# Kernel optimization log

Measured on AMD Instinct MI355X. Metric: run time of the kernel, lower is better.

## Reference

```python
import jax, jax.numpy as jnp
import numpy as np

B, C, H, W = 2, 320, 48, 48
HEADS, DIM_HEAD, NUM_FILTERS = 8, 64, 32
INNER = HEADS * DIM_HEAD  # 512
LN_EPS = 1e-05


def setup_inputs() -> dict:
    key = jax.random.key(0)
    ks = jax.random.split(key, 8)
    w = 0.02
    return {
        "hidden_states": jax.random.normal(ks[0], (B, C, H, W), jnp.float32),
        "encoder_hidden_states": jax.random.normal(ks[1], (B, C, H, W), jnp.float32),
        "Wq": jax.random.normal(ks[2], (C, INNER), jnp.float32) * w,
        "Wk": jax.random.normal(ks[3], (C, INNER), jnp.float32) * w,
        "Wv": jax.random.normal(ks[4], (C, INNER), jnp.float32) * w,
        "Wo": jax.random.normal(ks[5], (INNER, C), jnp.float32) * w,
        "bo": jnp.zeros((C,), jnp.float32),
        "ln_gamma": jnp.ones((C,), jnp.float32),
        "ln_beta": jnp.zeros((C,), jnp.float32),
        "ex_filters": jax.random.normal(ks[6], (NUM_FILTERS, INNER), jnp.float32),
        "dist_filters": jax.random.normal(ks[7], (NUM_FILTERS, INNER), jnp.float32),
        "scale": jnp.ones((1,), jnp.float32),  # learnable scale shadows dim_head**-0.5
    }


def _split_heads(t, heads):
    b, s, d = t.shape
    return t.reshape(b, s, heads, d // heads).transpose(0, 2, 1, 3)  # [b,h,s,dh]


def reference(hidden_states, encoder_hidden_states, Wq, Wk, Wv, Wo, bo,
              ln_gamma, ln_beta, ex_filters, dist_filters, scale):
    b, c, h, w = hidden_states.shape
    _, _, rh, rw = encoder_hidden_states.shape
    residual = hidden_states
    s = scale[0]

    hs = hidden_states.transpose(0, 2, 3, 1).reshape(b, h * w, c)        # [b, q, C]
    ehs = encoder_hidden_states.transpose(0, 2, 3, 1).reshape(b, rh * rw, c)

    # LayerNorm on encoder states
    mu = ehs.mean(-1, keepdims=True)
    var = jnp.mean((ehs - mu) ** 2, axis=-1, keepdims=True)
    ehs = (ehs - mu) * jax.lax.rsqrt(var + LN_EPS) * ln_gamma + ln_beta

    q = _split_heads(hs @ Wq, HEADS)    # [b,h,q,dh]
    k = _split_heads(ehs @ Wk, HEADS)   # [b,h,kv,dh]
    v = _split_heads(ehs @ Wv, HEADS)   # [b,h,kv,dh]
    ef = _split_heads(jnp.broadcast_to(ex_filters[None], (b,) + ex_filters.shape), HEADS)   # [b,h,F,dh]
    df = _split_heads(jnp.broadcast_to(dist_filters[None], (b,) + dist_filters.shape), HEADS)

    # spatial attention: softmax over kv positions
    spatial = jax.nn.softmax(jnp.einsum('bhfd,bhkd->bhfk', ef, k) * s, axis=-1)   # [b,h,F,kv]
    # channel attention: softmax over the filter axis (torch dim=1 of [B*h, F, q])
    channel = jax.nn.softmax(jnp.einsum('bhfd,bhqd->bhfq', df, q) * s, axis=2)    # [b,h,F,q]

    attn = jnp.einsum('bhfq,bhfk->bhqk', channel, spatial)                        # [b,h,q,kv]
    out = jnp.einsum('bhqk,bhkd->bhqd', attn, v)                                  # [b,h,q,dh]

    out = out.transpose(0, 2, 1, 3).reshape(b, h * w, INNER)
    out = out @ Wo + bo
    out = out.reshape(b, h, w, c).transpose(0, 3, 1, 2)
    return out + residual * s
```

## Files before the change

kernel.cpp:

```cpp
#include <hip/hip_runtime.h>
#include <math.h>

#define Bc 2
#define Cc 320
#define Pc 2304
#define HEADSc 8
#define DHc 64
#define INNERc 512
#define Fc 32
#define LN_EPS 1e-5f
#define CHUNKS 18
#define CHUNK_P 128

typedef __attribute__((ext_vector_type(8))) short bf16x8;
typedef __attribute__((ext_vector_type(4))) float f32x4;

static __device__ __forceinline__ ushort f2bf(float x) {
  uint u = __builtin_bit_cast(uint, x);
  u = (u + 0x7fffu + ((u >> 16) & 1u)) >> 16;
  return (ushort)u;
}

static __device__ __forceinline__ void gload16(const ushort* g, ushort* l) {
  __builtin_amdgcn_global_load_lds(
      (const __attribute__((address_space(1))) uint*)g,
      (__attribute__((address_space(3))) uint*)l, 16, 0, 0);
}

static __device__ void transpose_tile(const float* __restrict__ src,
                                      ushort* __restrict__ dst, int R, int C,
                                      int r0, int c0, int tid,
                                      float (*t)[65]) {
#pragma unroll
  for (int it = 0; it < 4; ++it) {
    int lin = it * 256 + tid;
    int rr = lin >> 4, c4 = lin & 15;
    float4 v = *(const float4*)(&src[(size_t)(r0 + rr) * C + c0 + c4 * 4]);
    t[rr][c4 * 4 + 0] = v.x; t[rr][c4 * 4 + 1] = v.y;
    t[rr][c4 * 4 + 2] = v.z; t[rr][c4 * 4 + 3] = v.w;
  }
  __syncthreads();
#pragma unroll
  for (int it = 0; it < 2; ++it) {
    int lin = it * 256 + tid;
    int cc = lin >> 3, r8 = lin & 7;
    ushort tmp[8];
#pragma unroll
    for (int j = 0; j < 8; ++j) tmp[j] = f2bf(t[r8 * 8 + j][cc]);
    *(uint4*)(&dst[(size_t)(c0 + cc) * R + r0 + r8 * 8]) = *(const uint4*)tmp;
  }
}

__global__ __launch_bounds__(256) void prep_all_kernel(
    const float* __restrict__ hs, const float* __restrict__ ehs,
    const float* __restrict__ gamma, const float* __restrict__ beta,
    const float* __restrict__ Wv, const float* __restrict__ Wo,
    const float* __restrict__ exf, const float* __restrict__ Wk,
    const float* __restrict__ dif, const float* __restrict__ Wq,
    ushort* __restrict__ hsT, ushort* __restrict__ ehsT,
    ushort* __restrict__ WvT, ushort* __restrict__ WoT,
    ushort* __restrict__ Gk, ushort* __restrict__ Gq) {
  __shared__ float smem[6448];
  int idx = blockIdx.x, tid = threadIdx.x;

  if (idx < 144) {
    int pt = idx % 36, z = idx / 36;
    int b = z & 1, which = z >> 1;
    int pos0 = pt * 64;
    const float* src = (which ? ehs : hs) + (size_t)b * Cc * Pc;
    ushort* dst = (which ? ehsT : hsT) + (size_t)b * Pc * Cc;
    float* t = smem;
    float* s1 = smem + 4160;
    float* s2 = smem + 4416;
    float* lmean = smem + 4672;
    float* lrstd = smem + 4736;
    int lane = tid & 63, g = tid >> 6;
    if (which) {
      const float* base = src + pos0 + lane;
      float sum = 0.f, sq = 0.f;
      for (int c = g * 80; c < g * 80 + 80; ++c) {
        float x = base[(size_t)c * Pc];
        sum += x; sq += x * x;
      }
      s1[g * 64 + lane] = sum; s2[g * 64 + lane] = sq;
      __syncthreads();
      if (tid < 64) {
        float ts = s1[tid] + s1[64 + tid] + s1[128 + tid] + s1[192 + tid];
        float tq = s2[tid] + s2[64 + tid] + s2[128 + tid] + s2[192 + tid];
        float mean = ts / (float)Cc;
        float var = tq / (float)Cc - mean * mean;
        lmean[tid] = mean;
        lrstd[tid] = rsqrtf(var + LN_EPS);
      }
      __syncthreads();
    }
    for (int ct = 0; ct < 5; ++ct) {
      int r0 = ct * 64;
#pragma unroll
      for (int it = 0; it < 4; ++it) {
        int lin = it * 256 + tid;
        int rr = lin >> 4, c4 = lin & 15;
        float4 v = *(const float4*)(&src[(size_t)(r0 + rr) * Pc + pos0 + c4 * 4]);
        t[rr * 65 + c4 * 4 + 0] = v.x; t[rr * 65 + c4 * 4 + 1] = v.y;
        t[rr * 65 + c4 * 4 + 2] = v.z; t[rr * 65 + c4 * 4 + 3] = v.w;
      }
      __syncthreads();
#pragma unroll
      for (int it = 0; it < 2; ++it) {
        int lin = it * 256 + tid;
        int cc = lin >> 3, r8 = lin & 7;
        float m_ = which ? lmean[cc] : 0.f, rs_ = which ? lrstd[cc] : 1.f;
        ushort tmp[8];
#pragma unroll
        for (int j = 0; j < 8; ++j) {
          int ch = r8 * 8 + j;
          float x = t[ch * 65 + cc];
          float val = which ? (x - m_) * rs_ * gamma[r0 + ch] + beta[r0 + ch] : x;
          tmp[j] = f2bf(val);
        }
        *(uint4*)(&dst[(size_t)(pos0 + cc) * Cc + r0 + r8 * 8]) =
            *(const uint4*)tmp;
      }
      __syncthreads();
    }
  } else {
    int idx2 = idx - 144;
    if (idx2 < 40) {
      transpose_tile(Wv, WvT, Cc, INNERc, (idx2 / 8) * 64, (idx2 % 8) * 64,
                     tid, (float(*)[65])smem);
    } else if (idx2 < 80) {
      int i = idx2 - 40;
      transpose_tile(Wo, WoT, INNERc, Cc, (i / 5) * 64, (i % 5) * 64, tid,
                     (float(*)[65])smem);
    } else {
      int i = idx2 - 80;
      int c0 = (i % 5) * 64, h = (i / 5) % 8, zz = i / 40;
      const float* filt = zz ? dif : exf;
      const float* W = zz ? Wq : Wk;
      ushort* G = zz ? Gq : Gk;
      float (*ef)[66] = (float(*)[66])smem;
      float (*wk)[65] = (float(*)[65])(smem + 32 * 66);
      for (int l = tid; l < Fc * DHc; l += 256) {
        int f = l >> 6, d = l & 63;
        ef[f][d] = filt[(size_t)f * INNERc + h * 64 + d];
      }
      for (int l = tid; l < 64 * DHc; l += 256) {
        int cc = l >> 6, d = l & 63;
        wk[cc][d] = W[(size_t)(c0 + cc) * INNERc + h * 64 + d];
      }
      __syncthreads();
      int f = tid >> 3, cbase = tid & 7;
      float acc[8] = {};
#pragma unroll
      for (int d4 = 0; d4 < DHc; d4 += 4) {
        float4 a = *(const float4*)(&ef[f][d4]);
#pragma unroll
        for (int j = 0; j < 8; ++j) {
          float4 b = *(const float4*)(&wk[cbase + j * 8][d4]);
          acc[j] += a.x * b.x + a.y * b.y + a.z * b.z + a.w * b.w;
        }
      }
#pragma unroll
      for (int j = 0; j < 8; ++j)
        G[(size_t)(h * Fc + f) * Cc + c0 + cbase + j * 8] = f2bf(acc[j]);
    }
  }
}

__global__ __launch_bounds__(256) void spatial_kernel(
    const ushort* __restrict__ Gk, const ushort* __restrict__ ehsT,
    const ushort* __restrict__ WvT, const float* __restrict__ scale_p,
    float* __restrict__ svp, float* __restrict__ mj, float* __restrict__ lj) {
  int c = blockIdx.x, h = blockIdx.y, b = blockIdx.z;
  int tid = threadIdx.x, lane = tid & 63, wv = tid >> 6;
  int l15 = lane & 15, kq = lane >> 4;
  int pos0 = c * CHUNK_P;
  int bh = b * HEADSc + h;
  float s = scale_p[0];

  __shared__ alignas(16) ushort As[96 * 64];
  __shared__ alignas(16) ushort Bs[128 * 64];
  __shared__ float Sq[32 * 132];
  __shared__ alignas(16) ushort P[32 * 136];
  __shared__ alignas(16) ushort Vs[64 * 136];

  const ushort* Av = WvT + (size_t)(h * 64) * Cc;
  const ushort* Ag = Gk + (size_t)(h * Fc) * Cc;
  const ushort* Bb = ehsT + ((size_t)b * Pc + pos0) * Cc;

  f32x4 acc[6][2] = {};
  for (int k0 = 0; k0 < Cc; k0 += 64) {
#pragma unroll
    for (int it = 0; it < 3; ++it) {
      int lin = it * 256 + tid;
      int row = lin >> 3, p = lin & 7;
      int lc = p ^ (row & 7);
      const ushort* sp = (row < 64) ? (Av + (size_t)row * Cc + k0 + lc * 8)
                                    : (Ag + (size_t)(row - 64) * Cc + k0 + lc * 8);
      gload16(sp, &As[lin * 8]);
    }
#pragma unroll
    for (int it = 0; it < 4; ++it) {
      int lin = it * 256 + tid;
      int row = lin >> 3, p = lin & 7;
      int lc = p ^ (row & 7);
      gload16(Bb + (size_t)row * Cc + k0 + lc * 8, &Bs[lin * 8]);
    }
    __syncthreads();
#pragma unroll
    for (int ss = 0; ss < 2; ++ss) {
      bf16x8 af[6], bfr[2];
#pragma unroll
      for (int mt = 0; mt < 6; ++mt) {
        int m = mt * 16 + l15;
        int p = (ss * 4 + kq) ^ (m & 7);
        af[mt] = *(const bf16x8*)(&As[m * 64 + p * 8]);
      }
#pragma unroll
      for (int nt = 0; nt < 2; ++nt) {
        int n = wv * 32 + nt * 16 + l15;
        int p = (ss * 4 + kq) ^ (n & 7);
        bfr[nt] = *(const bf16x8*)(&Bs[n * 64 + p * 8]);
      }
#pragma unroll
      for (int mt = 0; mt < 6; ++mt)
#pragma unroll
        for (int nt = 0; nt < 2; ++nt)
          acc[mt][nt] = __builtin_amdgcn_mfma_f32_16x16x32_bf16(
              af[mt], bfr[nt], acc[mt][nt], 0, 0, 0);
    }
    __syncthreads();
  }
#pragma unroll
  for (int mt = 0; mt < 6; ++mt)
#pragma unroll
    for (int nt = 0; nt < 2; ++nt) {
      int col = wv * 32 + nt * 16 + l15;
#pragma unroll
      for (int r = 0; r < 4; ++r) {
        int row = mt * 16 + kq * 4 + r;
        if (mt < 4) Vs[row * 136 + col] = f2bf(acc[mt][nt][r]);
        else Sq[(row - 64) * 132 + col] = acc[mt][nt][r];
      }
    }
  __syncthreads();

  {
    int row = tid >> 3, sub = tid & 7;
    float vals[16];
    float m_ = -1e30f;
#pragma unroll
    for (int i = 0; i < 16; ++i) {
      vals[i] = s * Sq[row * 132 + sub * 16 + i];
      m_ = fmaxf(m_, vals[i]);
    }
    m_ = fmaxf(m_, __shfl_xor(m_, 1));
    m_ = fmaxf(m_, __shfl_xor(m_, 2));
    m_ = fmaxf(m_, __shfl_xor(m_, 4));
    float l_ = 0.f;
#pragma unroll
    for (int i = 0; i < 16; i += 2) {
      float e0 = __expf(vals[i] - m_);
      float e1 = __expf(vals[i + 1] - m_);
      l_ += e0 + e1;
      uint pk = (uint)f2bf(e0) | ((uint)f2bf(e1) << 16);
      *(uint*)(&P[row * 136 + sub * 16 + i]) = pk;
    }
    l_ += __shfl_xor(l_, 1);
    l_ += __shfl_xor(l_, 2);
    l_ += __shfl_xor(l_, 4);
    if (sub == 0) {
      mj[((size_t)c * 16 + bh) * Fc + row] = m_;
      lj[((size_t)c * 16 + bh) * Fc + row] = l_;
    }
  }
  __syncthreads();

  f32x4 acc2[2] = {};
#pragma unroll
  for (int ss = 0; ss < 4; ++ss) {
    bf16x8 af[2];
#pragma unroll
    for (int mt = 0; mt < 2; ++mt)
      af[mt] = *(const bf16x8*)(&P[(mt * 16 + l15) * 136 + ss * 32 + kq * 8]);
    bf16x8 bfr = *(const bf16x8*)(&Vs[(wv * 16 + l15) * 136 + ss * 32 + kq * 8]);
#pragma unroll
    for (int mt = 0; mt < 2; ++mt)
      acc2[mt] = __builtin_amdgcn_mfma_f32_16x16x32_bf16(af[mt], bfr, acc2[mt],
                                                         0, 0, 0);
  }
  float* op = svp + ((size_t)c * 16 + bh) * (Fc * DHc);
#pragma unroll
  for (int mt = 0; mt < 2; ++mt)
#pragma unroll
    for (int r = 0; r < 4; ++r)
      op[(mt * 16 + kq * 4 + r) * DHc + wv * 16 + l15] = acc2[mt][r];
}

__global__ __launch_bounds__(256) void sv_reduce_kernel(
    const float* __restrict__ svp, const float* __restrict__ mj,
    const float* __restrict__ lj, ushort* __restrict__ svT) {
  int idx = blockIdx.x * 256 + threadIdx.x;
  int d = idx & 63, fr = idx >> 6;
  int bh = fr >> 5, f = fr & 31;
  float m = -1e30f;
#pragma unroll
  for (int c = 0; c < CHUNKS; ++c)
    m = fmaxf(m, mj[((size_t)c * 16 + bh) * Fc + f]);
  float osum = 0.f, lsum = 0.f;
#pragma unroll
  for (int c = 0; c < CHUNKS; ++c) {
    float w = __expf(mj[((size_t)c * 16 + bh) * Fc + f] - m);
    osum += w * svp[((size_t)c * 16 + bh) * (Fc * DHc) + f * DHc + d];
    lsum += w * lj[((size_t)c * 16 + bh) * Fc + f];
  }
  svT[((size_t)bh * DHc + d) * Fc + f] = f2bf(osum / lsum);
}

__global__ __launch_bounds__(256) void channel_kernel(
    const ushort* __restrict__ Gq, const ushort* __restrict__ hsT,
    const ushort* __restrict__ svT, const float* __restrict__ scale_p,
    ushort* __restrict__ OAT) {
  int pb = blockIdx.x, hp = blockIdx.y, b = blockIdx.z;
  int pos0 = pb * 64;
  int tid = threadIdx.x, lane = tid & 63, wv = tid >> 6;
  int l15 = lane & 15, kq = lane >> 4;
  float s = scale_p[0];

  __shared__ alignas(16) ushort Aq[2 * 32 * 64];
  __shared__ alignas(16) ushort Bs[64 * 64];
  __shared__ float SO[64 * 68];
  __shared__ alignas(16) ushort Pt[64 * 40];
  __shared__ alignas(16) ushort svs[64 * 40];
  __shared__ float red[4 * 64];

  f32x4 acc[2][2] = {};
  const ushort* Bb = hsT + ((size_t)b * Pc + pos0) * Cc;
  for (int k0 = 0; k0 < Cc; k0 += 64) {
#pragma unroll
    for (int it = 0; it < 2; ++it) {
      int lin = it * 256 + tid;
      int hh = lin >> 8, row = (lin >> 3) & 31, p = lin & 7;
      int lc = p ^ (row & 7);
      gload16(Gq + (size_t)((hp * 2 + hh) * Fc + row) * Cc + k0 + lc * 8,
              &Aq[lin * 8]);
    }
#pragma unroll
    for (int it = 0; it < 2; ++it) {
      int lin = it * 256 + tid;
      int row = lin >> 3, p = lin & 7;
      int lc = p ^ (row & 7);
      gload16(Bb + (size_t)row * Cc + k0 + lc * 8, &Bs[lin * 8]);
    }
    __syncthreads();
#pragma unroll
    for (int ss = 0; ss < 2; ++ss) {
      int n = wv * 16 + l15;
      int pb_ = (ss * 4 + kq) ^ (n & 7);
      bf16x8 bfr = *(const bf16x8*)(&Bs[n * 64 + pb_ * 8]);
#pragma unroll
      for (int hh = 0; hh < 2; ++hh)
#pragma unroll
        for (int mt = 0; mt < 2; ++mt) {
          int m = mt * 16 + l15;
          int pa = (ss * 4 + kq) ^ (m & 7);
          bf16x8 af = *(const bf16x8*)(&Aq[hh * 2048 + m * 64 + pa * 8]);
          acc[hh][mt] = __builtin_amdgcn_mfma_f32_16x16x32_bf16(
              af, bfr, acc[hh][mt], 0, 0, 0);
        }
    }
    __syncthreads();
  }

  for (int hh = 0; hh < 2; ++hh) {
    int h = hp * 2 + hh;
#pragma unroll
    for (int mt = 0; mt < 2; ++mt)
#pragma unroll
      for (int r = 0; r < 4; ++r)
        SO[(mt * 16 + kq * 4 + r) * 68 + wv * 16 + l15] = acc[hh][mt][r];
    {
      int rr = tid >> 2, p = tid & 3;
      *(uint4*)(&svs[rr * 40 + p * 8]) = *(const uint4*)(
          svT + ((size_t)(b * HEADSc + h) * DHc + rr) * Fc + p * 8);
    }
    __syncthreads();
    {
      int pos = tid & 63, g = tid >> 6;
      float v8[8];
      float pm = -1e30f;
#pragma unroll
      for (int i = 0; i < 8; ++i) {
        v8[i] = s * SO[(g * 8 + i) * 68 + pos];
        pm = fmaxf(pm, v8[i]);
      }
      red[g * 64 + pos] = pm;
      __syncthreads();
      float m_ = fmaxf(fmaxf(red[pos], red[64 + pos]),
                       fmaxf(red[128 + pos], red[192 + pos]));
      __syncthreads();
      float ps = 0.f;
#pragma unroll
      for (int i = 0; i < 8; ++i) {
        v8[i] = __expf(v8[i] - m_);
        ps += v8[i];
      }
      red[g * 64 + pos] = ps;
      __syncthreads();
      float inv = 1.f / (red[pos] + red[64 + pos] + red[128 + pos] +
                         red[192 + pos]);
#pragma unroll
      for (int i = 0; i < 8; i += 2) {
        uint pk = (uint)f2bf(v8[i] * inv) | ((uint)f2bf(v8[i + 1] * inv) << 16);
        *(uint*)(&Pt[pos * 40 + g * 8 + i]) = pk;
      }
    }
    __syncthreads();
    {
      bf16x8 b_ = *(const bf16x8*)(&svs[(wv * 16 + l15) * 40 + kq * 8]);
      f32x4 acc3[4];
#pragma unroll
      for (int mt = 0; mt < 4; ++mt) {
        bf16x8 a_ = *(const bf16x8*)(&Pt[(mt * 16 + l15) * 40 + kq * 8]);
        f32x4 z = {0.f, 0.f, 0.f, 0.f};
        acc3[mt] = __builtin_amdgcn_mfma_f32_16x16x32_bf16(a_, b_, z, 0, 0, 0);
      }
#pragma unroll
      for (int mt = 0; mt < 4; ++mt)
#pragma unroll
        for (int r = 0; r < 4; ++r)
          SO[(mt * 16 + kq * 4 + r) * 68 + wv * 16 + l15] = acc3[mt][r];
    }
    __syncthreads();
#pragma unroll
    for (int it = 0; it < 2; ++it) {
      int lin = it * 256 + tid;
      int p = lin >> 3, c8 = lin & 7;
      ushort tmp[8];
#pragma unroll
      for (int j = 0; j < 8; ++j) tmp[j] = f2bf(SO[p * 68 + c8 * 8 + j]);
      *(uint4*)(&OAT[((size_t)b * Pc + pos0 + p) * INNERc + h * 64 + c8 * 8]) =
          *(const uint4*)tmp;
    }
    __syncthreads();
  }
}

__global__ __launch_bounds__(256) void gemm_mfma_kernel(
    const ushort* __restrict__ A, const ushort* __restrict__ Bt,
    float* __restrict__ Out, int K, int Mdim,
    const float* __restrict__ bias, const float* __restrict__ res,
    const float* __restrict__ scale_p) {
  int b = blockIdx.z;
  int n0 = blockIdx.x * 128, m0 = blockIdx.y * 64;
  int tid = threadIdx.x, lane = tid & 63, wv = tid >> 6;
  int l15 = lane & 15, kq = lane >> 4;
  __shared__ alignas(16) ushort As[64 * 64];
  __shared__ alignas(16) ushort Bs[128 * 64];
  const ushort* Ab = A + (size_t)m0 * K;
  const ushort* Bb = Bt + ((size_t)b * Pc + n0) * K;

  f32x4 acc[4][2] = {};
  for (int k0 = 0; k0 < K; k0 += 64) {
#pragma unroll
    for (int it = 0; it < 2; ++it) {
      int lin = it * 256 + tid;
      int row = lin >> 3, p = lin & 7;
      int lc = p ^ (row & 7);
      gload16(Ab + (size_t)row * K + k0 + lc * 8, &As[lin * 8]);
    }
#pragma unroll
    for (int it = 0; it < 4; ++it) {
      int lin = it * 256 + tid;
      int row = lin >> 3, p = lin & 7;
      int lc = p ^ (row & 7);
      gload16(Bb + (size_t)row * K + k0 + lc * 8, &Bs[lin * 8]);
    }
    __syncthreads();
#pragma unroll
    for (int ss = 0; ss < 2; ++ss) {
      bf16x8 af[4], bfr[2];
#pragma unroll
      for (int mt = 0; mt < 4; ++mt) {
        int m = mt * 16 + l15;
        int p = (ss * 4 + kq) ^ (m & 7);
        af[mt] = *(const bf16x8*)(&As[m * 64 + p * 8]);
      }
#pragma unroll
      for (int nt = 0; nt < 2; ++nt) {
        int n = wv * 32 + nt * 16 + l15;
        int p = (ss * 4 + kq) ^ (n & 7);
        bfr[nt] = *(const bf16x8*)(&Bs[n * 64 + p * 8]);
      }
#pragma unroll
      for (int mt = 0; mt < 4; ++mt)
#pragma unroll
        for (int nt = 0; nt < 2; ++nt)
          acc[mt][nt] = __builtin_amdgcn_mfma_f32_16x16x32_bf16(
              af[mt], bfr[nt], acc[mt][nt], 0, 0, 0);
    }
    __syncthreads();
  }
  float s = scale_p[0];
  float* Ob = Out + ((size_t)b * Mdim + m0) * Pc + n0;
  const float* rb = res + ((size_t)b * Mdim + m0) * Pc + n0;
#pragma unroll
  for (int mt = 0; mt < 4; ++mt)
#pragma unroll
    for (int nt = 0; nt < 2; ++nt) {
      int ncol = wv * 32 + nt * 16 + l15;
#pragma unroll
      for (int r = 0; r < 4; ++r) {
        int m = mt * 16 + kq * 4 + r;
        Ob[(size_t)m * Pc + ncol] =
            acc[mt][nt][r] + bias[m0 + m] + s * rb[(size_t)m * Pc + ncol];
      }
    }
}

extern "C" void kernel_launch(void* const* d_in, const int* in_sizes, int n_in,
                              void* d_out, int out_size, void* d_ws, size_t ws_size,
                              hipStream_t stream) {
  const float* hs    = (const float*)d_in[0];
  const float* ehs   = (const float*)d_in[1];
  const float* Wq    = (const float*)d_in[2];
  const float* Wk    = (const float*)d_in[3];
  const float* Wv    = (const float*)d_in[4];
  const float* Wo    = (const float*)d_in[5];
  const float* bo    = (const float*)d_in[6];
  const float* gamma = (const float*)d_in[7];
  const float* beta  = (const float*)d_in[8];
  const float* exf   = (const float*)d_in[9];
  const float* dif   = (const float*)d_in[10];
  const float* scale = (const float*)d_in[11];
  float* out = (float*)d_out;

  float* ws = (float*)d_ws;
  float* svp = ws;
  float* mj  = svp + 589824;
  float* lj  = mj + 9216;
  ushort* hsT  = (ushort*)(lj + 9216);
  ushort* ehsT = hsT + 1474560;
  ushort* WvT  = ehsT + 1474560;
  ushort* WoT  = WvT + 163840;
  ushort* Gk   = WoT + 163840;
  ushort* Gq   = Gk + 81920;
  ushort* svT  = Gq + 81920;
  ushort* OAT  = svT + 32768;

  prep_all_kernel<<<dim3(304), dim3(256), 0, stream>>>(
      hs, ehs, gamma, beta, Wv, Wo, exf, Wk, dif, Wq,
      hsT, ehsT, WvT, WoT, Gk, Gq);
  spatial_kernel<<<dim3(CHUNKS, HEADSc, Bc), dim3(256), 0, stream>>>(
      Gk, ehsT, WvT, scale, svp, mj, lj);
  sv_reduce_kernel<<<dim3(128), dim3(256), 0, stream>>>(svp, mj, lj, svT);
  channel_kernel<<<dim3(Pc / 64, HEADSc / 2, Bc), dim3(256), 0, stream>>>(
      Gq, hsT, svT, scale, OAT);
  gemm_mfma_kernel<<<dim3(Pc / 128, Cc / 64, Bc), dim3(256), 0, stream>>>(
      WoT, OAT, out, INNERc, Cc, bo, hs, scale);
}
```

Baseline: 136.1 us.

## Shrink tiles across spatial, channel and output GEMM kernels to raise block counts

The spatial kernel now splits KV positions into 36 chunks of 64 instead of 18 of 128, and aliases its shared-memory buffers into one overlapping region to cut LDS use. The channel kernel processes one head per block instead of two, and the output GEMM uses 64-wide column tiles instead of 128. All three changes launch more, smaller blocks to fill the MI355X's many CUs better and raise occupancy. The cost is more partial results for the sv reduction, larger workspace, and less operand reuse per block.

```diff
diff --git a/kernel.cpp b/kernel.cpp
--- a/kernel.cpp
+++ b/kernel.cpp
@@ -9,8 +9,8 @@
 #define INNERc 512
 #define Fc 32
 #define LN_EPS 1e-5f
-#define CHUNKS 18
-#define CHUNK_P 128
+#define CHUNKS 36
+#define CHUNK_P 64
 
 typedef __attribute__((ext_vector_type(8))) short bf16x8;
 typedef __attribute__((ext_vector_type(4))) float f32x4;
@@ -178,17 +178,18 @@
   int bh = b * HEADSc + h;
   float s = scale_p[0];
 
-  __shared__ alignas(16) ushort As[96 * 64];
-  __shared__ alignas(16) ushort Bs[128 * 64];
-  __shared__ float Sq[32 * 132];
-  __shared__ alignas(16) ushort P[32 * 136];
-  __shared__ alignas(16) ushort Vs[64 * 136];
+  __shared__ alignas(16) char smem[22528];
+  ushort* As = (ushort*)smem;
+  ushort* Bs = (ushort*)(smem + 12288);
+  float* Sq = (float*)smem;
+  ushort* Vs = (ushort*)(smem + 8704);
+  ushort* P = (ushort*)(smem + 17920);
 
   const ushort* Av = WvT + (size_t)(h * 64) * Cc;
   const ushort* Ag = Gk + (size_t)(h * Fc) * Cc;
   const ushort* Bb = ehsT + ((size_t)b * Pc + pos0) * Cc;
 
-  f32x4 acc[6][2] = {};
+  f32x4 acc[6] = {};
   for (int k0 = 0; k0 < Cc; k0 += 64) {
 #pragma unroll
     for (int it = 0; it < 3; ++it) {
@@ -200,7 +201,7 @@
       gload16(sp, &As[lin * 8]);
     }
 #pragma unroll
-    for (int it = 0; it < 4; ++it) {
+    for (int it = 0; it < 2; ++it) {
       int lin = it * 256 + tid;
       int row = lin >> 3, p = lin & 7;
       int lc = p ^ (row & 7);
@@ -209,49 +210,44 @@
     __syncthreads();
 #pragma unroll
     for (int ss = 0; ss < 2; ++ss) {
-      bf16x8 af[6], bfr[2];
+      bf16x8 af[6], bfr;
 #pragma unroll
       for (int mt = 0; mt < 6; ++mt) {
         int m = mt * 16 + l15;
         int p = (ss * 4 + kq) ^ (m & 7);
         af[mt] = *(const bf16x8*)(&As[m * 64 + p * 8]);
       }
-#pragma unroll
-      for (int nt = 0; nt < 2; ++nt) {
-        int n = wv * 32 + nt * 16 + l15;
+      {
+        int n = wv * 16 + l15;
         int p = (ss * 4 + kq) ^ (n & 7);
-        bfr[nt] = *(const bf16x8*)(&Bs[n * 64 + p * 8]);
+        bfr = *(const bf16x8*)(&Bs[n * 64 + p * 8]);
       }
 #pragma unroll
       for (int mt = 0; mt < 6; ++mt)
-#pragma unroll
-        for (int nt = 0; nt < 2; ++nt)
-          acc[mt][nt] = __builtin_amdgcn_mfma_f32_16x16x32_bf16(
-              af[mt], bfr[nt], acc[mt][nt], 0, 0, 0);
-    }
-    __syncthreads();
-  }
-#pragma unroll
-  for (int mt = 0; mt < 6; ++mt)
-#pragma unroll
-    for (int nt = 0; nt < 2; ++nt) {
-      int col = wv * 32 + nt * 16 + l15;
-#pragma unroll
-      for (int r = 0; r < 4; ++r) {
-        int row = mt * 16 + kq * 4 + r;
-        if (mt < 4) Vs[row * 136 + col] = f2bf(acc[mt][nt][r]);
-        else Sq[(row - 64) * 132 + col] = acc[mt][nt][r];
-      }
-    }
+        acc[mt] = __builtin_amdgcn_mfma_f32_16x16x32_bf16(af[mt], bfr, acc[mt],
+                                                          0, 0, 0);
+    }
+    __syncthreads();
+  }
+#pragma unroll
+  for (int mt = 0; mt < 6; ++mt) {
+    int col = wv * 16 + l15;
+#pragma unroll
+    for (int r = 0; r < 4; ++r) {
+      int row = mt * 16 + kq * 4 + r;
+      if (mt < 4) Vs[row * 72 + col] = f2bf(acc[mt][r]);
+      else Sq[(row - 64) * 68 + col] = acc[mt][r];
+    }
+  }
   __syncthreads();
 
   {
     int row = tid >> 3, sub = tid & 7;
-    float vals[16];
+    float vals[8];
     float m_ = -1e30f;
 #pragma unroll
-    for (int i = 0; i < 16; ++i) {
-      vals[i] = s * Sq[row * 132 + sub * 16 + i];
+    for (int i = 0; i < 8; ++i) {
+      vals[i] = s * Sq[row * 68 + sub * 8 + i];
       m_ = fmaxf(m_, vals[i]);
     }
     m_ = fmaxf(m_, __shfl_xor(m_, 1));
@@ -259,12 +255,12 @@
     m_ = fmaxf(m_, __shfl_xor(m_, 4));
     float l_ = 0.f;
 #pragma unroll
-    for (int i = 0; i < 16; i += 2) {
+    for (int i = 0; i < 8; i += 2) {
       float e0 = __expf(vals[i] - m_);
       float e1 = __expf(vals[i + 1] - m_);
       l_ += e0 + e1;
       uint pk = (uint)f2bf(e0) | ((uint)f2bf(e1) << 16);
-      *(uint*)(&P[row * 136 + sub * 16 + i]) = pk;
+      *(uint*)(&P[row * 72 + sub * 8 + i]) = pk;
     }
     l_ += __shfl_xor(l_, 1);
     l_ += __shfl_xor(l_, 2);
@@ -278,12 +274,12 @@
 
   f32x4 acc2[2] = {};
 #pragma unroll
-  for (int ss = 0; ss < 4; ++ss) {
+  for (int ss = 0; ss < 2; ++ss) {
     bf16x8 af[2];
 #pragma unroll
     for (int mt = 0; mt < 2; ++mt)
-      af[mt] = *(const bf16x8*)(&P[(mt * 16 + l15) * 136 + ss * 32 + kq * 8]);
-    bf16x8 bfr = *(const bf16x8*)(&Vs[(wv * 16 + l15) * 136 + ss * 32 + kq * 8]);
+      af[mt] = *(const bf16x8*)(&P[(mt * 16 + l15) * 72 + ss * 32 + kq * 8]);
+    bf16x8 bfr = *(const bf16x8*)(&Vs[(wv * 16 + l15) * 72 + ss * 32 + kq * 8]);
 #pragma unroll
     for (int mt = 0; mt < 2; ++mt)
       acc2[mt] = __builtin_amdgcn_mfma_f32_16x16x32_bf16(af[mt], bfr, acc2[mt],
@@ -308,7 +304,7 @@
   for (int c = 0; c < CHUNKS; ++c)
     m = fmaxf(m, mj[((size_t)c * 16 + bh) * Fc + f]);
   float osum = 0.f, lsum = 0.f;
-#pragma unroll
+#pragma unroll 4
   for (int c = 0; c < CHUNKS; ++c) {
     float w = __expf(mj[((size_t)c * 16 + bh) * Fc + f] - m);
     osum += w * svp[((size_t)c * 16 + bh) * (Fc * DHc) + f * DHc + d];
@@ -321,29 +317,29 @@
     const ushort* __restrict__ Gq, const ushort* __restrict__ hsT,
     const ushort* __restrict__ svT, const float* __restrict__ scale_p,
     ushort* __restrict__ OAT) {
-  int pb = blockIdx.x, hp = blockIdx.y, b = blockIdx.z;
+  int pb = blockIdx.x, h = blockIdx.y, b = blockIdx.z;
   int pos0 = pb * 64;
   int tid = threadIdx.x, lane = tid & 63, wv = tid >> 6;
   int l15 = lane & 15, kq = lane >> 4;
   float s = scale_p[0];
 
-  __shared__ alignas(16) ushort Aq[2 * 32 * 64];
-  __shared__ alignas(16) ushort Bs[64 * 64];
-  __shared__ float SO[64 * 68];
-  __shared__ alignas(16) ushort Pt[64 * 40];
-  __shared__ alignas(16) ushort svs[64 * 40];
-  __shared__ float red[4 * 64];
-
-  f32x4 acc[2][2] = {};
+  __shared__ alignas(16) char smem[28672];
+  ushort* Aq = (ushort*)smem;
+  ushort* Bs = (ushort*)(smem + 4096);
+  float* SO = (float*)smem;
+  ushort* Pt = (ushort*)(smem + 17408);
+  ushort* svs = (ushort*)(smem + 22528);
+  float* red = (float*)(smem + 27648);
+
+  f32x4 acc[2] = {};
   const ushort* Bb = hsT + ((size_t)b * Pc + pos0) * Cc;
+  const ushort* Ab = Gq + (size_t)(h * Fc) * Cc;
   for (int k0 = 0; k0 < Cc; k0 += 64) {
-#pragma unroll
-    for (int it = 0; it < 2; ++it) {
-      int lin = it * 256 + tid;
-      int hh = lin >> 8, row = (lin >> 3) & 31, p = lin & 7;
+    {
+      int lin = tid;
+      int row = lin >> 3, p = lin & 7;
       int lc = p ^ (row & 7);
-      gload16(Gq + (size_t)((hp * 2 + hh) * Fc + row) * Cc + k0 + lc * 8,
-              &Aq[lin * 8]);
+      gload16(Ab + (size_t)row * Cc + k0 + lc * 8, &Aq[lin * 8]);
     }
 #pragma unroll
     for (int it = 0; it < 2; ++it) {
@@ -359,90 +355,84 @@
       int pb_ = (ss * 4 + kq) ^ (n & 7);
       bf16x8 bfr = *(const bf16x8*)(&Bs[n * 64 + pb_ * 8]);
 #pragma unroll
-      for (int hh = 0; hh < 2; ++hh)
-#pragma unroll
-        for (int mt = 0; mt < 2; ++mt) {
-          int m = mt * 16 + l15;
-          int pa = (ss * 4 + kq) ^ (m & 7);
-          bf16x8 af = *(const bf16x8*)(&Aq[hh * 2048 + m * 64 + pa * 8]);
-          acc[hh][mt] = __builtin_amdgcn_mfma_f32_16x16x32_bf16(
-              af, bfr, acc[hh][mt], 0, 0, 0);
-        }
-    }
-    __syncthreads();
-  }
-
-  for (int hh = 0; hh < 2; ++hh) {
-    int h = hp * 2 + hh;
-#pragma unroll
-    for (int mt = 0; mt < 2; ++mt)
+      for (int mt = 0; mt < 2; ++mt) {
+        int m = mt * 16 + l15;
+        int pa = (ss * 4 + kq) ^ (m & 7);
+        bf16x8 af = *(const bf16x8*)(&Aq[m * 64 + pa * 8]);
+        acc[mt] = __builtin_amdgcn_mfma_f32_16x16x32_bf16(af, bfr, acc[mt],
+                                                          0, 0, 0);
+      }
+    }
+    __syncthreads();
+  }
+
+#pragma unroll
+  for (int mt = 0; mt < 2; ++mt)
+#pragma unroll
+    for (int r = 0; r < 4; ++r)
+      SO[(mt * 16 + kq * 4 + r) * 68 + wv * 16 + l15] = acc[mt][r];
+  {
+    int rr = tid >> 2, p = tid & 3;
+    *(uint4*)(&svs[rr * 40 + p * 8]) = *(const uint4*)(
+        svT + ((size_t)(b * HEADSc + h) * DHc + rr) * Fc + p * 8);
+  }
+  __syncthreads();
+  {
+    int pos = tid & 63, g = tid >> 6;
+    float v8[8];
+    float pm = -1e30f;
+#pragma unroll
+    for (int i = 0; i < 8; ++i) {
+      v8[i] = s * SO[(g * 8 + i) * 68 + pos];
+      pm = fmaxf(pm, v8[i]);
+    }
+    red[g * 64 + pos] = pm;
+    __syncthreads();
+    float m_ = fmaxf(fmaxf(red[pos], red[64 + pos]),
+                     fmaxf(red[128 + pos], red[192 + pos]));
+    __syncthreads();
+    float ps = 0.f;
+#pragma unroll
+    for (int i = 0; i < 8; ++i) {
+      v8[i] = __expf(v8[i] - m_);
+      ps += v8[i];
+    }
+    red[g * 64 + pos] = ps;
+    __syncthreads();
+    float inv = 1.f / (red[pos] + red[64 + pos] + red[128 + pos] +
+                       red[192 + pos]);
+#pragma unroll
+    for (int i = 0; i < 8; i += 2) {
+      uint pk = (uint)f2bf(v8[i] * inv) | ((uint)f2bf(v8[i + 1] * inv) << 16);
+      *(uint*)(&Pt[pos * 40 + g * 8 + i]) = pk;
+    }
+  }
+  __syncthreads();
+  {
+    bf16x8 b_ = *(const bf16x8*)(&svs[(wv * 16 + l15) * 40 + kq * 8]);
+    f32x4 acc3[4];
+#pragma unroll
+    for (int mt = 0; mt < 4; ++mt) {
+      bf16x8 a_ = *(const bf16x8*)(&Pt[(mt * 16 + l15) * 40 + kq * 8]);
+      f32x4 z = {0.f, 0.f, 0.f, 0.f};
+      acc3[mt] = __builtin_amdgcn_mfma_f32_16x16x32_bf16(a_, b_, z, 0, 0, 0);
+    }
+#pragma unroll
+    for (int mt = 0; mt < 4; ++mt)
 #pragma unroll
       for (int r = 0; r < 4; ++r)
-        SO[(mt * 16 + kq * 4 + r) * 68 + wv * 16 + l15] = acc[hh][mt][r];
-    {
-      int rr = tid >> 2, p = tid & 3;
-      *(uint4*)(&svs[rr * 40 + p * 8]) = *(const uint4*)(
-          svT + ((size_t)(b * HEADSc + h) * DHc + rr) * Fc + p * 8);
-    }
-    __syncthreads();
-    {
-      int pos = tid & 63, g = tid >> 6;
-      float v8[8];
-      float pm = -1e30f;
-#pragma unroll
-      for (int i = 0; i < 8; ++i) {
-        v8[i] = s * SO[(g * 8 + i) * 68 + pos];
-        pm = fmaxf(pm, v8[i]);
-      }
-      red[g * 64 + pos] = pm;
-      __syncthreads();
-      float m_ = fmaxf(fmaxf(red[pos], red[64 + pos]),
-                       fmaxf(red[128 + pos], red[192 + pos]));
-      __syncthreads();
-      float ps = 0.f;
-#pragma unroll
-      for (int i = 0; i < 8; ++i) {
-        v8[i] = __expf(v8[i] - m_);
-        ps += v8[i];
-      }
-      red[g * 64 + pos] = ps;
-      __syncthreads();
-      float inv = 1.f / (red[pos] + red[64 + pos] + red[128 + pos] +
-                         red[192 + pos]);
-#pragma unroll
-      for (int i = 0; i < 8; i += 2) {
-        uint pk = (uint)f2bf(v8[i] * inv) | ((uint)f2bf(v8[i + 1] * inv) << 16);
-        *(uint*)(&Pt[pos * 40 + g * 8 + i]) = pk;
-      }
-    }
-    __syncthreads();
-    {
-      bf16x8 b_ = *(const bf16x8*)(&svs[(wv * 16 + l15) * 40 + kq * 8]);
-      f32x4 acc3[4];
-#pragma unroll
-      for (int mt = 0; mt < 4; ++mt) {
-        bf16x8 a_ = *(const bf16x8*)(&Pt[(mt * 16 + l15) * 40 + kq * 8]);
-        f32x4 z = {0.f, 0.f, 0.f, 0.f};
-        acc3[mt] = __builtin_amdgcn_mfma_f32_16x16x32_bf16(a_, b_, z, 0, 0, 0);
-      }
-#pragma unroll
-      for (int mt = 0; mt < 4; ++mt)
-#pragma unroll
-        for (int r = 0; r < 4; ++r)
-          SO[(mt * 16 + kq * 4 + r) * 68 + wv * 16 + l15] = acc3[mt][r];
-    }
-    __syncthreads();
-#pragma unroll
-    for (int it = 0; it < 2; ++it) {
-      int lin = it * 256 + tid;
-      int p = lin >> 3, c8 = lin & 7;
-      ushort tmp[8];
-#pragma unroll
-      for (int j = 0; j < 8; ++j) tmp[j] = f2bf(SO[p * 68 + c8 * 8 + j]);
-      *(uint4*)(&OAT[((size_t)b * Pc + pos0 + p) * INNERc + h * 64 + c8 * 8]) =
-          *(const uint4*)tmp;
-    }
-    __syncthreads();
+        SO[(mt * 16 + kq * 4 + r) * 68 + wv * 16 + l15] = acc3[mt][r];
+  }
+  __syncthreads();
+#pragma unroll
+  for (int it = 0; it < 2; ++it) {
+    int lin = it * 256 + tid;
+    int p = lin >> 3, c8 = lin & 7;
+    ushort tmp[8];
+#pragma unroll
+    for (int j = 0; j < 8; ++j) tmp[j] = f2bf(SO[p * 68 + c8 * 8 + j]);
+    *(uint4*)(&OAT[((size_t)b * Pc + pos0 + p) * INNERc + h * 64 + c8 * 8]) =
+        *(const uint4*)tmp;
   }
 }
 
@@ -452,15 +442,15 @@
     const float* __restrict__ bias, const float* __restrict__ res,
     const float* __restrict__ scale_p) {
   int b = blockIdx.z;
-  int n0 = blockIdx.x * 128, m0 = blockIdx.y * 64;
+  int n0 = blockIdx.x * 64, m0 = blockIdx.y * 64;
   int tid = threadIdx.x, lane = tid & 63, wv = tid >> 6;
   int l15 = lane & 15, kq = lane >> 4;
   __shared__ alignas(16) ushort As[64 * 64];
-  __shared__ alignas(16) ushort Bs[128 * 64];
+  __shared__ alignas(16) ushort Bs[64 * 64];
   const ushort* Ab = A + (size_t)m0 * K;
   const ushort* Bb = Bt + ((size_t)b * Pc + n0) * K;
 
-  f32x4 acc[4][2] = {};
+  f32x4 acc[4] = {};
   for (int k0 = 0; k0 < K; k0 += 64) {
 #pragma unroll
     for (int it = 0; it < 2; ++it) {
@@ -470,7 +460,7 @@
       gload16(Ab + (size_t)row * K + k0 + lc * 8, &As[lin * 8]);
     }
 #pragma unroll
-    for (int it = 0; it < 4; ++it) {
+    for (int it = 0; it < 2; ++it) {
       int lin = it * 256 + tid;
       int row = lin >> 3, p = lin & 7;
       int lc = p ^ (row & 7);
@@ -479,42 +469,36 @@
     __syncthreads();
 #pragma unroll
     for (int ss = 0; ss < 2; ++ss) {
-      bf16x8 af[4], bfr[2];
+      bf16x8 af[4], bfr;
 #pragma unroll
       for (int mt = 0; mt < 4; ++mt) {
         int m = mt * 16 + l15;
         int p = (ss * 4 + kq) ^ (m & 7);
         af[mt] = *(const bf16x8*)(&As[m * 64 + p * 8]);
       }
-#pragma unroll
-      for (int nt = 0; nt < 2; ++nt) {
-        int n = wv * 32 + nt * 16 + l15;
+      {
+        int n = wv * 16 + l15;
         int p = (ss * 4 + kq) ^ (n & 7);
-        bfr[nt] = *(const bf16x8*)(&Bs[n * 64 + p * 8]);
+        bfr = *(const bf16x8*)(&Bs[n * 64 + p * 8]);
       }
 #pragma unroll
       for (int mt = 0; mt < 4; ++mt)
-#pragma unroll
-        for (int nt = 0; nt < 2; ++nt)
-          acc[mt][nt] = __builtin_amdgcn_mfma_f32_16x16x32_bf16(
-              af[mt], bfr[nt], acc[mt][nt], 0, 0, 0);
+        acc[mt] = __builtin_amdgcn_mfma_f32_16x16x32_bf16(af[mt], bfr, acc[mt],
+                                                          0, 0, 0);
     }
     __syncthreads();
   }
   float s = scale_p[0];
   float* Ob = Out + ((size_t)b * Mdim + m0) * Pc + n0;
   const float* rb = res + ((size_t)b * Mdim + m0) * Pc + n0;
+  int ncol = wv * 16 + l15;
 #pragma unroll
   for (int mt = 0; mt < 4; ++mt)
 #pragma unroll
-    for (int nt = 0; nt < 2; ++nt) {
-      int ncol = wv * 32 + nt * 16 + l15;
-#pragma unroll
-      for (int r = 0; r < 4; ++r) {
-        int m = mt * 16 + kq * 4 + r;
-        Ob[(size_t)m * Pc + ncol] =
-            acc[mt][nt][r] + bias[m0 + m] + s * rb[(size_t)m * Pc + ncol];
-      }
+    for (int r = 0; r < 4; ++r) {
+      int m = mt * 16 + kq * 4 + r;
+      Ob[(size_t)m * Pc + ncol] =
+          acc[mt][r] + bias[m0 + m] + s * rb[(size_t)m * Pc + ncol];
     }
 }
 
@@ -537,9 +521,9 @@
 
   float* ws = (float*)d_ws;
   float* svp = ws;
-  float* mj  = svp + 589824;
-  float* lj  = mj + 9216;
-  ushort* hsT  = (ushort*)(lj + 9216);
+  float* mj  = svp + 1179648;
+  float* lj  = mj + 18432;
+  ushort* hsT  = (ushort*)(lj + 18432);
   ushort* ehsT = hsT + 1474560;
   ushort* WvT  = ehsT + 1474560;
   ushort* WoT  = WvT + 163840;
@@ -554,8 +538,8 @@
   spatial_kernel<<<dim3(CHUNKS, HEADSc, Bc), dim3(256), 0, stream>>>(
       Gk, ehsT, WvT, scale, svp, mj, lj);
   sv_reduce_kernel<<<dim3(128), dim3(256), 0, stream>>>(svp, mj, lj, svT);
-  channel_kernel<<<dim3(Pc / 64, HEADSc / 2, Bc), dim3(256), 0, stream>>>(
+  channel_kernel<<<dim3(Pc / 64, HEADSc, Bc), dim3(256), 0, stream>>>(
       Gq, hsT, svT, scale, OAT);
-  gemm_mfma_kernel<<<dim3(Pc / 128, Cc / 64, Bc), dim3(256), 0, stream>>>(
+  gemm_mfma_kernel<<<dim3(Pc / 64, Cc / 64, Bc), dim3(256), 0, stream>>>(
       WoT, OAT, out, INNERc, Cc, bo, hs, scale);
 }
```

Result: faster. 133.2 us (-2.1%).
